# Kernel optimization log

Measured on AMD Instinct MI355X. Metric: run time of the kernel, lower is better.

The kernel has to match this reference:

```python
import jax
import jax.numpy as jnp
import numpy as np

K = 32            # sparsity
MAX_ITERS = 8     # max_iterations
TOL = 1e-6        # tolerance
M, N, B = 1024, 4096, 16
SMAX = 2 * K * MAX_ITERS  # support grows by <= 2K per iter, never pruned mid-run


def setup_inputs() -> dict:
    key = jax.random.key(0)
    k1, k2 = jax.random.split(key)
    A = jax.random.normal(k1, (M, N), dtype=jnp.float32) / np.float32(np.sqrt(M))
    measurements = jax.random.normal(k2, (B, M), dtype=jnp.float32)
    return {"measurements": measurements, "A": A}


def _cosamp_single(A, y, k, max_iters, tol, smax):
    m, n = A.shape
    dtype = A.dtype

    def step(state, _):
        x, support, residual, done = state
        # signal proxy; note torch's proxy[support] = -abs(proxy[support]) is a
        # no-op under the subsequent topk(abs(proxy)) and is faithfully omitted.
        proxy = A.T @ residual                                   # [n]
        _, omega = jax.lax.top_k(jnp.abs(proxy), 2 * k)          # [2k]
        support_new = support.at[omega].set(True)                # [n] bool
        # gather support columns into a fixed-size slot set (stable sort: True first)
        idx = jnp.argsort(~support_new)[:smax]                   # [smax]
        valid = support_new[idx]                                 # [smax] bool
        A_sub = A[:, idx] * valid[None, :].astype(dtype)         # [m, smax], padding cols zeroed
        # least squares over support columns via normal equations
        # (A_sub full column rank since |support| <= smax < m); identity on
        # padding slots keeps G invertible and forces their coeffs to 0.
        G = A_sub.T @ A_sub + jnp.diag(jnp.where(valid, 0.0, 1.0).astype(dtype))
        sol = jnp.linalg.solve(G, A_sub.T @ y) * valid.astype(dtype)
        x_dense = jnp.zeros(n, dtype).at[idx].set(sol)           # scatter back to [n]
        # hard threshold to k largest magnitudes
        _, tid = jax.lax.top_k(jnp.abs(x_dense), k)
        x_new = jnp.zeros(n, dtype).at[tid].set(x_dense[tid])
        r_new = y - A @ x_new
        conv = jnp.linalg.norm(r_new) < tol
        sup_conv = jnp.zeros(n, bool).at[tid].set(True)
        nsup = jnp.where(conv, sup_conv, support_new)
        # freeze state after convergence (emulates the torch early break)
        x_out = jnp.where(done, x, x_new)
        sup_out = jnp.where(done, support, nsup)
        r_out = jnp.where(done, residual, r_new)
        return (x_out, sup_out, r_out, done | conv), None

    init = (jnp.zeros(n, dtype), jnp.zeros(n, bool), y, jnp.array(False))
    (x, _, _, _), _ = jax.lax.scan(step, init, None, length=max_iters)
    return x


def reference(measurements, A):
    # vmap CoSaMP across the batch (torch loops over b in Python)
    run = jax.vmap(lambda y: _cosamp_single(A, y, K, MAX_ITERS, TOL, SMAX))
    return run(measurements)  # [B, N]
```

## Files before the change

### kernel.cpp

```cpp
#include <hip/hip_runtime.h>
#include <cstdint>
#include <cstddef>

#define Mdim 1024
#define Ndim 4096
#define Bdim 16
#define SMax 512
#define K2v  64
#define KKv  32
#define NIT  8
#define PQ   8

__global__ __launch_bounds__(256) void k_init(const float* __restrict__ Y, float* __restrict__ Rres,
        int* __restrict__ Flags, int* __restrict__ Sold, int* __restrict__ Snew, int* __restrict__ Done){
  int idx = blockIdx.x * 256 + threadIdx.x;
  int total = Bdim * Ndim;
  for (int t = idx; t < total; t += gridDim.x * 256){
    Flags[t] = 0;
    if (t < Bdim * Mdim) Rres[t] = Y[t];
    if (t < Bdim){ Sold[t] = 0; Snew[t] = 0; Done[t] = 0; }
  }
}

__global__ __launch_bounds__(256) void k_transpose(const float* __restrict__ A, float* __restrict__ At){
  __shared__ float tile[32][33];
  int j0 = blockIdx.x * 32, i0 = blockIdx.y * 32;
  int tx = threadIdx.x, ty = threadIdx.y;
  for (int r = 0; r < 32; r += 8)
    tile[ty + r][tx] = A[(size_t)(i0 + ty + r) * Ndim + (j0 + tx)];
  __syncthreads();
  for (int r = 0; r < 32; r += 8)
    At[(size_t)(j0 + ty + r) * Mdim + (i0 + tx)] = tile[tx][ty + r];
}

__global__ __launch_bounds__(256) void k_proxy(const float* __restrict__ A, const float* __restrict__ Rres,
        float* __restrict__ PP){
  int j = blockIdx.x * 256 + threadIdx.x;
  int rq = blockIdx.y;
  __shared__ float Rq[Bdim][128];
  for (int e = threadIdx.x; e < Bdim * 128; e += 256){
    int b = e >> 7, i = e & 127;
    Rq[b][i] = Rres[b * Mdim + rq * 128 + i];
  }
  __syncthreads();
  float acc[Bdim];
  #pragma unroll
  for (int b = 0; b < Bdim; ++b) acc[b] = 0.0f;
  for (int i = 0; i < 128; ++i){
    float a = A[(size_t)(rq * 128 + i) * Ndim + j];
    #pragma unroll
    for (int b = 0; b < Bdim; ++b) acc[b] = fmaf(a, Rq[b][i], acc[b]);
  }
  #pragma unroll
  for (int b = 0; b < Bdim; ++b)
    PP[(size_t)(rq * Bdim + b) * Ndim + j] = acc[b];
}

__global__ __launch_bounds__(1024) void k_topk(const float* __restrict__ PP, int* __restrict__ Flags,
        int* __restrict__ Cols, int* __restrict__ Sold, int* __restrict__ Snew, const int* __restrict__ Done){
  int b = blockIdx.x;
  if (Done[b]) return;
  __shared__ unsigned long long keys[Ndim];
  int tid = threadIdx.x;
  for (int j = tid; j < Ndim; j += 1024){
    float v = 0.0f;
    #pragma unroll
    for (int q = 0; q < PQ; ++q) v += PP[(size_t)(q * Bdim + b) * Ndim + j];
    unsigned int ab = __float_as_uint(fabsf(v));
    keys[j] = ((unsigned long long)ab << 32) | (unsigned int)j;
  }
  __syncthreads();
  for (int ksz = 2; ksz <= Ndim; ksz <<= 1){
    for (int jsz = ksz >> 1; jsz > 0; jsz >>= 1){
      for (int t = tid; t < Ndim / 2; t += 1024){
        int i = 2 * t - (t & (jsz - 1));
        int ixj = i ^ jsz;
        unsigned long long a = keys[i], c = keys[ixj];
        bool sw = ((i & ksz) == 0) ? (a < c) : (a > c);
        if (sw){ keys[i] = c; keys[ixj] = a; }
      }
      __syncthreads();
    }
  }
  if (tid < 64){
    int s = Snew[b];
    if (tid == 0) Sold[b] = s;
    int j = (int)(keys[tid] & 0xFFFFFFFFu);
    int notin = (Flags[b * Ndim + j] == 0) ? 1 : 0;
    unsigned long long bal = __ballot(notin);
    if (notin){
      int pos = s + __popcll(bal & ((1ull << tid) - 1ull));
      Flags[b * Ndim + j] = 1;
      Cols[b * SMax + pos] = j;
    }
    if (tid == 0) Snew[b] = s + (int)__popcll(bal);
  }
}

__global__ __launch_bounds__(256) void k_gram(const float* __restrict__ At, const float* __restrict__ Y,
        float* __restrict__ G, float* __restrict__ Bv,
        const int* __restrict__ Cols, const int* __restrict__ Sold, const int* __restrict__ Snew,
        const int* __restrict__ Done){
  int b = blockIdx.x;
  if (Done[b]) return;
  int s0 = Sold[b], s1 = Snew[b];
  int p0 = s0 + (int)blockIdx.y * 4;
  if (p0 >= s1) return;
  int np = min(4, s1 - p0);
  __shared__ float Ap[4][Mdim];
  int tid = threadIdx.x;
  for (int e = tid; e < 4 * Mdim; e += 256){
    int pi = e >> 10, i = e & (Mdim - 1);
    Ap[pi][i] = (p0 + pi < s1) ? At[(size_t)Cols[b * SMax + p0 + pi] * Mdim + i] : 0.0f;
  }
  __syncthreads();
  int w = tid >> 6, lane = tid & 63;
  for (int q = w; q <= s1; q += 4){
    const float* aq = (q < s1) ? (At + (size_t)Cols[b * SMax + q] * Mdim) : (Y + (size_t)b * Mdim);
    float a0 = 0, a1 = 0, a2 = 0, a3 = 0;
    #pragma unroll
    for (int c = 0; c < 16; ++c){
      float v = aq[lane + 64 * c];
      a0 = fmaf(v, Ap[0][lane + 64 * c], a0);
      a1 = fmaf(v, Ap[1][lane + 64 * c], a1);
      a2 = fmaf(v, Ap[2][lane + 64 * c], a2);
      a3 = fmaf(v, Ap[3][lane + 64 * c], a3);
    }
    #pragma unroll
    for (int off = 32; off > 0; off >>= 1){
      a0 += __shfl_xor(a0, off);
      a1 += __shfl_xor(a1, off);
      a2 += __shfl_xor(a2, off);
      a3 += __shfl_xor(a3, off);
    }
    if (lane == 0){
      float av[4] = {a0, a1, a2, a3};
      for (int r = 0; r < np; ++r){
        int p = p0 + r;
        if (q < s1){
          G[((size_t)b * SMax + p) * SMax + q] = av[r];
          G[((size_t)b * SMax + q) * SMax + p] = av[r];
        } else {
          Bv[(size_t)b * SMax + p] = av[r];
        }
      }
    }
  }
}

__global__ __launch_bounds__(256) void k_V(const float* __restrict__ G, const float* __restrict__ Gi,
        float* __restrict__ V, const int* __restrict__ Sold, const int* __restrict__ Snew,
        const int* __restrict__ Done){
  int b = blockIdx.x;
  if (Done[b]) return;
  int s0 = Sold[b], s1 = Snew[b], nn = s1 - s0;
  int i0 = (int)blockIdx.y * 64;
  if (i0 >= s0) return;
  __shared__ float Gt[64][65];
  __shared__ float Bt[64][65];
  int tid = threadIdx.x;
  int tx = tid & 15, ty = tid >> 4;
  float acc[4][4];
  #pragma unroll
  for (int r = 0; r < 4; ++r)
    #pragma unroll
    for (int c = 0; c < 4; ++c) acc[r][c] = 0.0f;
  for (int k0 = 0; k0 < s0; k0 += 64){
    for (int e = tid; e < 64 * 64; e += 256){
      int r = e >> 6, c = e & 63;
      Gt[r][c] = Gi[((size_t)b * SMax + i0 + r) * SMax + k0 + c];
      Bt[r][c] = (k0 + r < s0 && c < nn) ? G[((size_t)b * SMax + k0 + r) * SMax + s0 + c] : 0.0f;
    }
    __syncthreads();
    for (int d = 0; d < 64; ++d){
      float gv[4], bv[4];
      #pragma unroll
      for (int r = 0; r < 4; ++r) gv[r] = Gt[ty * 4 + r][d];
      #pragma unroll
      for (int c = 0; c < 4; ++c) bv[c] = Bt[d][tx * 4 + c];
      #pragma unroll
      for (int r = 0; r < 4; ++r)
        #pragma unroll
        for (int c = 0; c < 4; ++c) acc[r][c] = fmaf(gv[r], bv[c], acc[r][c]);
    }
    __syncthreads();
  }
  for (int r = 0; r < 4; ++r)
    for (int c = 0; c < 4; ++c){
      int i = i0 + ty * 4 + r, cc = tx * 4 + c;
      if (i < s0 && cc < nn)
        V[((size_t)b * SMax + i) * K2v + cc] = acc[r][c];
    }
}

template<int J, int I> struct RowU {
  static __device__ __forceinline__ void go(float (&s)[64], float (&w)[64]){
    if constexpr (I != J){
      float f = __uint_as_float((unsigned)__builtin_amdgcn_readlane((int)__float_as_uint(s[I]), J));
      s[I] = fmaf(-f, s[J], s[I]);
      w[I] = fmaf(-f, w[J], w[I]);
    }
    if constexpr (I + 1 < 64) RowU<J, I + 1>::go(s, w);
  }
};
template<int J> struct PivT {
  static __device__ __forceinline__ void go(float (&s)[64], float (&w)[64]){
    float d = __uint_as_float((unsigned)__builtin_amdgcn_readlane((int)__float_as_uint(s[J]), J));
    float rp = 1.0f / d;
    s[J] *= rp;
    w[J] *= rp;
    RowU<J, 0>::go(s, w);
    if constexpr (J + 1 < 64) PivT<J + 1>::go(s, w);
  }
};

__global__ __launch_bounds__(256, 1) void k_schur(const float* __restrict__ G, const float* __restrict__ V,
        float* __restrict__ Si, const int* __restrict__ Sold, const int* __restrict__ Snew,
        const int* __restrict__ Done){
  int b = blockIdx.x;
  if (Done[b]) return;
  int s0 = Sold[b], s1 = Snew[b], nn = s1 - s0;
  __shared__ float Sm[64][65];
  __shared__ float Bt[64][65];
  __shared__ float Vt[64][65];
  int tid = threadIdx.x;
  int tx = tid & 15, ty = tid >> 4;
  float acc[4][4];
  #pragma unroll
  for (int r = 0; r < 4; ++r)
    #pragma unroll
    for (int c = 0; c < 4; ++c) acc[r][c] = 0.0f;
  for (int k0 = 0; k0 < s0; k0 += 64){
    for (int e = tid; e < 64 * 64; e += 256){
      int r = e >> 6, c = e & 63;
      bool ok = (k0 + r < s0) && (c < nn);
      Bt[r][c] = ok ? G[((size_t)b * SMax + k0 + r) * SMax + s0 + c] : 0.0f;
      Vt[r][c] = ok ? V[((size_t)b * SMax + k0 + r) * K2v + c] : 0.0f;
    }
    __syncthreads();
    for (int d = 0; d < 64; ++d){
      float bm[4], vv[4];
      #pragma unroll
      for (int r = 0; r < 4; ++r) bm[r] = Bt[d][ty * 4 + r];
      #pragma unroll
      for (int c = 0; c < 4; ++c) vv[c] = Vt[d][tx * 4 + c];
      #pragma unroll
      for (int r = 0; r < 4; ++r)
        #pragma unroll
        for (int c = 0; c < 4; ++c) acc[r][c] = fmaf(bm[r], vv[c], acc[r][c]);
    }
    __syncthreads();
  }
  for (int r = 0; r < 4; ++r)
    for (int c = 0; c < 4; ++c){
      int rr = ty * 4 + r, cc = tx * 4 + c;
      float sval;
      if (rr < nn && cc < nn)
        sval = G[((size_t)b * SMax + s0 + rr) * SMax + s0 + cc] - acc[r][c];
      else
        sval = (rr == cc) ? 1.0f : 0.0f;
      Sm[rr][cc] = sval;
    }
  __syncthreads();
  if (tid < 64){
    float s[64], w[64];
    #pragma unroll
    for (int r = 0; r < 64; ++r){
      s[r] = Sm[r][tid];
      w[r] = (r == tid) ? 1.0f : 0.0f;
    }
    PivT<0>::go(s, w);
    #pragma unroll
    for (int r = 0; r < 64; ++r)
      Si[(size_t)b * K2v * K2v + r * K2v + tid] = w[r];
  }
}

__global__ __launch_bounds__(256) void k_T(const float* __restrict__ V, const float* __restrict__ Si,
        float* __restrict__ T, const int* __restrict__ Sold, const int* __restrict__ Snew,
        const int* __restrict__ Done){
  int b = blockIdx.x;
  if (Done[b]) return;
  int s0 = Sold[b], s1 = Snew[b], nn = s1 - s0;
  int i0 = (int)blockIdx.y * 64;
  if (i0 >= s0) return;
  __shared__ float Vt[64][65];
  __shared__ float Ss[64][65];
  int tid = threadIdx.x;
  for (int e = tid; e < 64 * 64; e += 256){
    int r = e >> 6, c = e & 63;
    Vt[r][c] = (i0 + r < s0 && c < nn) ? V[((size_t)b * SMax + i0 + r) * K2v + c] : 0.0f;
    Ss[r][c] = Si[(size_t)b * K2v * K2v + e];
  }
  __syncthreads();
  int tx = tid & 15, ty = tid >> 4;
  float acc[4][4];
  #pragma unroll
  for (int r = 0; r < 4; ++r)
    #pragma unroll
    for (int c = 0; c < 4; ++c) acc[r][c] = 0.0f;
  for (int d = 0; d < 64; ++d){
    float vv[4], sv[4];
    #pragma unroll
    for (int r = 0; r < 4; ++r) vv[r] = Vt[ty * 4 + r][d];
    #pragma unroll
    for (int c = 0; c < 4; ++c) sv[c] = Ss[d][tx * 4 + c];
    #pragma unroll
    for (int r = 0; r < 4; ++r)
      #pragma unroll
      for (int c = 0; c < 4; ++c) acc[r][c] = fmaf(vv[r], sv[c], acc[r][c]);
  }
  for (int r = 0; r < 4; ++r)
    for (int c = 0; c < 4; ++c){
      int i = i0 + ty * 4 + r, dd = tx * 4 + c;
      if (i < s0 && dd < nn)
        T[((size_t)b * SMax + i) * K2v + dd] = acc[r][c];
    }
}

__global__ __launch_bounds__(256) void k_upd(float* __restrict__ Gi, const float* __restrict__ T,
        const float* __restrict__ V, const float* __restrict__ Si,
        const int* __restrict__ Sold, const int* __restrict__ Snew, const int* __restrict__ Done){
  int b = blockIdx.x;
  if (Done[b]) return;
  int s0 = Sold[b], s1 = Snew[b];
  int i0 = (int)blockIdx.y * 64, k0 = (int)blockIdx.z * 64;
  if (i0 >= s1 || k0 >= s1) return;
  int nn = s1 - s0;
  __shared__ float Tt[64][65];
  __shared__ float Vk[64][65];
  __shared__ float Tk[64][65];
  int tid = threadIdx.x;
  for (int e = tid; e < 64 * 64; e += 256){
    int r = e >> 6, c = e & 63;
    Tt[r][c] = (i0 + r < s0 && c < nn) ? T[((size_t)b * SMax + i0 + r) * K2v + c] : 0.0f;
    Tk[r][c] = (k0 + r < s0 && c < nn) ? T[((size_t)b * SMax + k0 + r) * K2v + c] : 0.0f;
    Vk[r][c] = (k0 + r < s0 && c < nn) ? V[((size_t)b * SMax + k0 + r) * K2v + c] : 0.0f;
  }
  __syncthreads();
  int tx = tid & 15, ty = tid >> 4;
  float acc[4][4];
  #pragma unroll
  for (int r = 0; r < 4; ++r)
    #pragma unroll
    for (int c = 0; c < 4; ++c) acc[r][c] = 0.0f;
  for (int d = 0; d < 64; ++d){
    float tv[4], vv[4];
    #pragma unroll
    for (int r = 0; r < 4; ++r) tv[r] = Tt[ty * 4 + r][d];
    #pragma unroll
    for (int c = 0; c < 4; ++c) vv[c] = Vk[tx * 4 + c][d];
    #pragma unroll
    for (int r = 0; r < 4; ++r)
      #pragma unroll
      for (int c = 0; c < 4; ++c) acc[r][c] = fmaf(tv[r], vv[c], acc[r][c]);
  }
  for (int r = 0; r < 4; ++r)
    for (int c = 0; c < 4; ++c){
      int i = i0 + ty * 4 + r, k = k0 + tx * 4 + c;
      if (i < s1 && k < s1){
        size_t idx = ((size_t)b * SMax + i) * SMax + k;
        float val;
        if (i < s0){
          if (k < s0) val = Gi[idx] + acc[r][c];
          else        val = -Tt[ty * 4 + r][k - s0];
        } else {
          if (k < s0) val = -Tk[tx * 4 + c][i - s0];
          else        val = Si[(size_t)b * K2v * K2v + (i - s0) * K2v + (k - s0)];
        }
        Gi[idx] = val;
      }
    }
}

__global__ __launch_bounds__(256) void k_gemv(const float* __restrict__ Mat, const float* __restrict__ vecsrc,
        const float* __restrict__ addsrc, float* __restrict__ out, float sgn,
        const int* __restrict__ Snew, const int* __restrict__ Done){
  int b = blockIdx.x;
  if (Done[b]) return;
  int s1 = Snew[b];
  int i0 = (int)blockIdx.y * 64;
  if (i0 >= s1) return;
  __shared__ float vs[SMax];
  int tid = threadIdx.x;
  int w = tid >> 6, lane = tid & 63;
  vs[tid]       = (tid < s1)       ? vecsrc[(size_t)b * SMax + tid]       : 0.0f;
  vs[tid + 256] = (tid + 256 < s1) ? vecsrc[(size_t)b * SMax + tid + 256] : 0.0f;
  __syncthreads();
  #pragma unroll
  for (int g = 0; g < 4; ++g){
    int base = i0 + w * 16 + g * 4;
    if (base >= s1) break;
    const float* p0 = Mat + ((size_t)b * SMax + base) * SMax;
    const float* p1 = Mat + ((size_t)b * SMax + (base + 1 < s1 ? base + 1 : base)) * SMax;
    const float* p2 = Mat + ((size_t)b * SMax + (base + 2 < s1 ? base + 2 : base)) * SMax;
    const float* p3 = Mat + ((size_t)b * SMax + (base + 3 < s1 ? base + 3 : base)) * SMax;
    float a0 = 0, a1 = 0, a2 = 0, a3 = 0;
    #pragma unroll
    for (int c = 0; c < 8; ++c){
      int idx = lane + 64 * c;
      float v = vs[idx];
      a0 = fmaf(p0[idx], v, a0);
      a1 = fmaf(p1[idx], v, a1);
      a2 = fmaf(p2[idx], v, a2);
      a3 = fmaf(p3[idx], v, a3);
    }
    #pragma unroll
    for (int off = 32; off > 0; off >>= 1){
      a0 += __shfl_xor(a0, off); a1 += __shfl_xor(a1, off);
      a2 += __shfl_xor(a2, off); a3 += __shfl_xor(a3, off);
    }
    if (lane == 0){
      float av[4] = {a0, a1, a2, a3};
      #pragma unroll
      for (int r = 0; r < 4; ++r){
        int i = base + r;
        if (i < s1)
          out[(size_t)b * SMax + i] = sgn * av[r] + (addsrc ? addsrc[(size_t)b * SMax + i] : 0.0f);
      }
    }
  }
}

__global__ __launch_bounds__(1024) void k_finish(const float* __restrict__ Zz, const float* __restrict__ At,
        const float* __restrict__ Y, const int* __restrict__ Cols, const int* __restrict__ Snew,
        int* __restrict__ Done, float* __restrict__ XKval, int* __restrict__ XKcol, float* __restrict__ Rres){
  int b = blockIdx.x;
  if (Done[b]) return;
  int s1 = Snew[b];
  __shared__ unsigned long long sk[SMax];
  __shared__ float xv[KKv];
  __shared__ int   xc[KKv];
  __shared__ float red[16];
  int tid = threadIdx.x;
  if (tid < SMax){
    unsigned long long key = 0;
    if (tid < s1){
      float z = Zz[(size_t)b * SMax + tid];
      unsigned int ab = __float_as_uint(fabsf(z));
      int col = Cols[b * SMax + tid];
      key = ((unsigned long long)ab << 32) | ((unsigned long long)(4095 - col) << 20) | (unsigned int)tid;
    }
    sk[tid] = key;
  }
  __syncthreads();
  for (int ksz = 2; ksz <= SMax; ksz <<= 1){
    for (int jsz = ksz >> 1; jsz > 0; jsz >>= 1){
      for (int t = tid; t < SMax / 2; t += 1024){
        int i = 2 * t - (t & (jsz - 1));
        int ixj = i ^ jsz;
        unsigned long long a = sk[i], c = sk[ixj];
        bool sw = ((i & ksz) == 0) ? (a < c) : (a > c);
        if (sw){ sk[i] = c; sk[ixj] = a; }
      }
      __syncthreads();
    }
  }
  if (tid < KKv){
    unsigned long long key = sk[tid];
    int p = (int)(key & 0xFFFFFu);
    float v = Zz[(size_t)b * SMax + p];
    xv[tid] = v;
    xc[tid] = Cols[b * SMax + p];
    XKval[b * KKv + tid] = v;
    XKcol[b * KKv + tid] = xc[tid];
  }
  __syncthreads();
  float r = Y[(size_t)b * Mdim + tid];
  for (int t = 0; t < KKv; ++t)
    r = fmaf(-xv[t], At[(size_t)xc[t] * Mdim + tid], r);
  Rres[(size_t)b * Mdim + tid] = r;
  float ss = r * r;
  #pragma unroll
  for (int off = 32; off > 0; off >>= 1) ss += __shfl_xor(ss, off);
  if ((tid & 63) == 0) red[tid >> 6] = ss;
  __syncthreads();
  if (tid == 0){
    float tot = 0;
    for (int w = 0; w < 16; ++w) tot += red[w];
    if (tot < 1e-12f) Done[b] = 1;
  }
}

__global__ __launch_bounds__(1024) void k_output(const float* __restrict__ XKval, const int* __restrict__ XKcol,
        float* __restrict__ out){
  int b = blockIdx.x;
  __shared__ float xv[KKv];
  __shared__ int   xc[KKv];
  if (threadIdx.x < KKv){
    xv[threadIdx.x] = XKval[b * KKv + threadIdx.x];
    xc[threadIdx.x] = XKcol[b * KKv + threadIdx.x];
  }
  __syncthreads();
  int j = blockIdx.y * 1024 + threadIdx.x;
  float v = 0.0f;
  #pragma unroll
  for (int t = 0; t < KKv; ++t) v = (xc[t] == j) ? xv[t] : v;
  out[(size_t)b * Ndim + j] = v;
}

extern "C" void kernel_launch(void* const* d_in, const int* in_sizes, int n_in,
                              void* d_out, int out_size, void* d_ws, size_t ws_size,
                              hipStream_t stream){
  const float* Y = (const float*)d_in[0];
  const float* A = (const float*)d_in[1];
  float* ws = (float*)d_ws;
  size_t off = 0;
  float* At   = ws + off; off += (size_t)Ndim * Mdim;
  float* G    = ws + off; off += (size_t)Bdim * SMax * SMax;
  float* Gi   = ws + off; off += (size_t)Bdim * SMax * SMax;
  float* V    = ws + off; off += (size_t)Bdim * SMax * K2v;
  float* T    = ws + off; off += (size_t)Bdim * SMax * K2v;
  float* Si   = ws + off; off += (size_t)Bdim * K2v * K2v;
  float* PP   = ws + off; off += (size_t)PQ * Bdim * Ndim;
  float* Rres = ws + off; off += (size_t)Bdim * Mdim;
  float* Bv   = ws + off; off += (size_t)Bdim * SMax;
  float* Z0   = ws + off; off += (size_t)Bdim * SMax;
  float* R2   = ws + off; off += (size_t)Bdim * SMax;
  float* Zz   = ws + off; off += (size_t)Bdim * SMax;
  float* XKval = ws + off; off += (size_t)Bdim * KKv;
  int* XKcol = (int*)(ws + off); off += (size_t)Bdim * KKv;
  int* Cols  = (int*)(ws + off); off += (size_t)Bdim * SMax;
  int* Flags = (int*)(ws + off); off += (size_t)Bdim * Ndim;
  int* Sold  = (int*)(ws + off); off += Bdim;
  int* Snew  = (int*)(ws + off); off += Bdim;
  int* Done  = (int*)(ws + off); off += Bdim;

  k_init<<<256, 256, 0, stream>>>(Y, Rres, Flags, Sold, Snew, Done);
  k_transpose<<<dim3(Ndim / 32, Mdim / 32), dim3(32, 8), 0, stream>>>(A, At);
  for (int t = 0; t < NIT; ++t){
    k_proxy<<<dim3(Ndim / 256, PQ), 256, 0, stream>>>(A, Rres, PP);
    k_topk<<<Bdim, 1024, 0, stream>>>(PP, Flags, Cols, Sold, Snew, Done);
    k_gram<<<dim3(Bdim, 16), 256, 0, stream>>>(At, Y, G, Bv, Cols, Sold, Snew, Done);
    if (t > 0)
      k_V<<<dim3(Bdim, t), 256, 0, stream>>>(G, Gi, V, Sold, Snew, Done);
    k_schur<<<Bdim, 256, 0, stream>>>(G, V, Si, Sold, Snew, Done);
    if (t > 0)
      k_T<<<dim3(Bdim, t), 256, 0, stream>>>(V, Si, T, Sold, Snew, Done);
    k_upd<<<dim3(Bdim, t + 1, t + 1), 256, 0, stream>>>(Gi, T, V, Si, Sold, Snew, Done);
    k_gemv<<<dim3(Bdim, 8), 256, 0, stream>>>(Gi, Bv, nullptr, Z0, 1.0f, Snew, Done);
    k_gemv<<<dim3(Bdim, 8), 256, 0, stream>>>(G, Z0, Bv, R2, -1.0f, Snew, Done);
    k_gemv<<<dim3(Bdim, 8), 256, 0, stream>>>(Gi, R2, Z0, Zz, 1.0f, Snew, Done);
    k_finish<<<Bdim, 1024, 0, stream>>>(Zz, At, Y, Cols, Snew, Done, XKval, XKcol, Rres);
  }
  k_output<<<dim3(Bdim, Ndim / 1024), 1024, 0, stream>>>(XKval, XKcol, (float*)d_out);
}
```

Before: 1.833 ms.

## Parallelize Schur complement product across tiles and split gram columns over z-dimension

The product B^T V inside the Schur complement, which was previously accumulated serially over k-tiles by a single block per batch, moves into a new kernel k_S. k_S launches one block per 64-row tile and writes partial products into the reused PP buffer, and k_schur then sums those partials before the 64x64 inversion. The gram kernel also gets a z-dimension of 2 so each block handles every other group of q columns, doubling the number of blocks. The aim is more parallelism on lightly occupied kernels, at the cost of an extra launch and a round trip of partial sums through global memory.

```diff
diff --git a/kernel.cpp b/kernel.cpp
--- a/kernel.cpp
+++ b/kernel.cpp
@@ -115,7 +115,7 @@
   }
   __syncthreads();
   int w = tid >> 6, lane = tid & 63;
-  for (int q = w; q <= s1; q += 4){
+  for (int q = 4 * (int)blockIdx.z + w; q <= s1; q += 8){
     const float* aq = (q < s1) ? (At + (size_t)Cols[b * SMax + q] * Mdim) : (Y + (size_t)b * Mdim);
     float a0 = 0, a1 = 0, a2 = 0, a3 = 0;
     #pragma unroll
@@ -193,6 +193,49 @@
     }
 }
 
+__global__ __launch_bounds__(256) void k_S(const float* __restrict__ G, const float* __restrict__ V,
+        float* __restrict__ SP, const int* __restrict__ Sold, const int* __restrict__ Snew,
+        const int* __restrict__ Done){
+  int b = blockIdx.x;
+  if (Done[b]) return;
+  int s0 = Sold[b], s1 = Snew[b], nn = s1 - s0;
+  int k0 = (int)blockIdx.y * 64;
+  if (k0 >= s0) return;
+  __shared__ float Bt[64][65];
+  __shared__ float Vt[64][65];
+  int tid = threadIdx.x;
+  int tx = tid & 15, ty = tid >> 4;
+  for (int e = tid; e < 64 * 64; e += 256){
+    int r = e >> 6, c = e & 63;
+    bool ok = (k0 + r < s0) && (c < nn);
+    Bt[r][c] = ok ? G[((size_t)b * SMax + k0 + r) * SMax + s0 + c] : 0.0f;
+    Vt[r][c] = ok ? V[((size_t)b * SMax + k0 + r) * K2v + c] : 0.0f;
+  }
+  __syncthreads();
+  float acc[4][4];
+  #pragma unroll
+  for (int r = 0; r < 4; ++r)
+    #pragma unroll
+    for (int c = 0; c < 4; ++c) acc[r][c] = 0.0f;
+  for (int d = 0; d < 64; ++d){
+    float bm[4], vv[4];
+    #pragma unroll
+    for (int r = 0; r < 4; ++r) bm[r] = Bt[d][ty * 4 + r];
+    #pragma unroll
+    for (int c = 0; c < 4; ++c) vv[c] = Vt[d][tx * 4 + c];
+    #pragma unroll
+    for (int r = 0; r < 4; ++r)
+      #pragma unroll
+      for (int c = 0; c < 4; ++c) acc[r][c] = fmaf(bm[r], vv[c], acc[r][c]);
+  }
+  float* dst = SP + ((size_t)(b * 8 + (int)blockIdx.y)) * 4096;
+  #pragma unroll
+  for (int r = 0; r < 4; ++r)
+    #pragma unroll
+    for (int c = 0; c < 4; ++c)
+      dst[(ty * 4 + r) * 64 + tx * 4 + c] = acc[r][c];
+}
+
 template<int J, int I> struct RowU {
   static __device__ __forceinline__ void go(float (&s)[64], float (&w)[64]){
     if constexpr (I != J){
@@ -214,53 +257,27 @@
   }
 };
 
-__global__ __launch_bounds__(256, 1) void k_schur(const float* __restrict__ G, const float* __restrict__ V,
+__global__ __launch_bounds__(256, 1) void k_schur(const float* __restrict__ G, const float* __restrict__ SP,
         float* __restrict__ Si, const int* __restrict__ Sold, const int* __restrict__ Snew,
         const int* __restrict__ Done){
   int b = blockIdx.x;
   if (Done[b]) return;
   int s0 = Sold[b], s1 = Snew[b], nn = s1 - s0;
+  int ntiles = (s0 + 63) >> 6;
   __shared__ float Sm[64][65];
-  __shared__ float Bt[64][65];
-  __shared__ float Vt[64][65];
-  int tid = threadIdx.x;
-  int tx = tid & 15, ty = tid >> 4;
-  float acc[4][4];
-  #pragma unroll
-  for (int r = 0; r < 4; ++r)
-    #pragma unroll
-    for (int c = 0; c < 4; ++c) acc[r][c] = 0.0f;
-  for (int k0 = 0; k0 < s0; k0 += 64){
-    for (int e = tid; e < 64 * 64; e += 256){
-      int r = e >> 6, c = e & 63;
-      bool ok = (k0 + r < s0) && (c < nn);
-      Bt[r][c] = ok ? G[((size_t)b * SMax + k0 + r) * SMax + s0 + c] : 0.0f;
-      Vt[r][c] = ok ? V[((size_t)b * SMax + k0 + r) * K2v + c] : 0.0f;
-    }
-    __syncthreads();
-    for (int d = 0; d < 64; ++d){
-      float bm[4], vv[4];
-      #pragma unroll
-      for (int r = 0; r < 4; ++r) bm[r] = Bt[d][ty * 4 + r];
-      #pragma unroll
-      for (int c = 0; c < 4; ++c) vv[c] = Vt[d][tx * 4 + c];
-      #pragma unroll
-      for (int r = 0; r < 4; ++r)
-        #pragma unroll
-        for (int c = 0; c < 4; ++c) acc[r][c] = fmaf(bm[r], vv[c], acc[r][c]);
-    }
-    __syncthreads();
-  }
-  for (int r = 0; r < 4; ++r)
-    for (int c = 0; c < 4; ++c){
-      int rr = ty * 4 + r, cc = tx * 4 + c;
-      float sval;
-      if (rr < nn && cc < nn)
-        sval = G[((size_t)b * SMax + s0 + rr) * SMax + s0 + cc] - acc[r][c];
-      else
-        sval = (rr == cc) ? 1.0f : 0.0f;
-      Sm[rr][cc] = sval;
-    }
+  int tid = threadIdx.x;
+  for (int e = tid; e < 4096; e += 256){
+    int rr = e >> 6, cc = e & 63;
+    float sval;
+    if (rr < nn && cc < nn){
+      sval = G[((size_t)b * SMax + s0 + rr) * SMax + s0 + cc];
+      for (int t = 0; t < ntiles; ++t)
+        sval -= SP[((size_t)(b * 8 + t)) * 4096 + e];
+    } else {
+      sval = (rr == cc) ? 1.0f : 0.0f;
+    }
+    Sm[rr][cc] = sval;
+  }
   __syncthreads();
   if (tid < 64){
     float s[64], w[64];
@@ -525,16 +542,19 @@
   int* Sold  = (int*)(ws + off); off += Bdim;
   int* Snew  = (int*)(ws + off); off += Bdim;
   int* Done  = (int*)(ws + off); off += Bdim;
+  float* SP = PP;
 
   k_init<<<256, 256, 0, stream>>>(Y, Rres, Flags, Sold, Snew, Done);
   k_transpose<<<dim3(Ndim / 32, Mdim / 32), dim3(32, 8), 0, stream>>>(A, At);
   for (int t = 0; t < NIT; ++t){
     k_proxy<<<dim3(Ndim / 256, PQ), 256, 0, stream>>>(A, Rres, PP);
     k_topk<<<Bdim, 1024, 0, stream>>>(PP, Flags, Cols, Sold, Snew, Done);
-    k_gram<<<dim3(Bdim, 16), 256, 0, stream>>>(At, Y, G, Bv, Cols, Sold, Snew, Done);
-    if (t > 0)
+    k_gram<<<dim3(Bdim, 16, 2), 256, 0, stream>>>(At, Y, G, Bv, Cols, Sold, Snew, Done);
+    if (t > 0){
       k_V<<<dim3(Bdim, t), 256, 0, stream>>>(G, Gi, V, Sold, Snew, Done);
-    k_schur<<<Bdim, 256, 0, stream>>>(G, V, Si, Sold, Snew, Done);
+      k_S<<<dim3(Bdim, t), 256, 0, stream>>>(G, V, SP, Sold, Snew, Done);
+    }
+    k_schur<<<Bdim, 256, 0, stream>>>(G, SP, Si, Sold, Snew, Done);
     if (t > 0)
       k_T<<<dim3(Bdim, t), 256, 0, stream>>>(V, Si, T, Sold, Snew, Done);
     k_upd<<<dim3(Bdim, t + 1, t + 1), 256, 0, stream>>>(Gi, T, V, Si, Sold, Snew, Done);
```

New measurement: 1.702 ms. -7.1%, faster.
